# Kernel optimization log

Measured on AMD Instinct MI355X. Metric: run time of the kernel, lower is better.

## Reference

```python
import jax, jax.numpy as jnp
import numpy as np

WINDOW = 1024
HOP = 256

def setup_inputs() -> dict:
    key = jax.random.key(0)
    X = jax.random.normal(key, (16, 2, 262144), dtype=jnp.float32)
    return {"X": X}

def reference(X):
    # X: (B, 2, T) with channel 0 = Re, channel 1 = Im.
    # Identity-weight Conv1d(1, window, kernel=window, stride=hop) is exactly
    # strided framing: frame t is X[..., t*hop : t*hop + window].
    B, _, T = X.shape
    n_frames = (T - WINDOW) // HOP + 1
    # (n_frames, WINDOW) gather index into the time axis
    idx = jnp.arange(n_frames)[:, None] * HOP + jnp.arange(WINDOW)[None, :]
    frames = X[:, :, idx]                      # (B, 2, n_frames, WINDOW)
    return jnp.transpose(frames, (0, 1, 3, 2)) # (B, 2, WINDOW, n_frames)
```

## Files before the change

kernel.cpp:

```cpp
#include <hip/hip_runtime.h>

#define WINDOW_SZ 1024
#define HOP_SZ    256
#define NFRAMES   1021
#define T_LEN     262144

#define FT 256
#define WT 16
#define LDS_S 261

__global__ __launch_bounds__(256)
void frame_transpose2(const float* __restrict__ X, float* __restrict__ out) {
    __shared__ __align__(16) float lds[WT * LDS_S];

    const int tid  = threadIdx.x;
    const int f0   = blockIdx.x * FT;
    const int w0   = blockIdx.y * WT;
    const int bc   = blockIdx.z;
    const int flim = min(FT, NFRAMES - f0);

    const float* Xb = X + (size_t)bc * T_LEN;

    {
        const int q  = tid & 3;
        const int fr = tid >> 2;
#pragma unroll
        for (int p = 0; p < 4; ++p) {
            const int f = fr + 64 * p;
            if (f < flim) {
                const float4 v = *(const float4*)(Xb + (size_t)(f0 + f) * HOP_SZ + w0 + 4 * q);
                float* dst = &lds[(4 * q) * LDS_S + f];
                dst[0 * LDS_S] = v.x;
                dst[1 * LDS_S] = v.y;
                dst[2 * LDS_S] = v.z;
                dst[3 * LDS_S] = v.w;
            }
        }
    }
    __syncthreads();

    {
        const int lane = tid & 63;
        const int wv   = tid >> 6;
#pragma unroll
        for (int i = 0; i < 4; ++i) {
            const int wl = wv * 4 + i;
            const int wg = w0 + wl;
            const int p  = (4 - (wg & 3)) & 3;
            float* orow = out + ((size_t)bc * WINDOW_SZ + wg) * (size_t)NFRAMES + f0;
            const float* lrow = &lds[wl * LDS_S];

            const int fv = p + 4 * lane;
            if (fv + 4 <= flim) {
                const float4 v = *(const float4*)(lrow + fv);
                *(float4*)(orow + fv) = v;
            }
            const int nt = (flim - p) & 3;
            const int ts = flim - nt;
            int fs = -1;
            if (lane < p) fs = lane;
            else if (lane < p + nt) fs = ts + (lane - p);
            if (fs >= 0) orow[fs] = lrow[fs];
        }
    }
}

extern "C" void kernel_launch(void* const* d_in, const int* in_sizes, int n_in,
                              void* d_out, int out_size, void* d_ws, size_t ws_size,
                              hipStream_t stream) {
    const float* X = (const float*)d_in[0];
    float* out = (float*)d_out;

    dim3 block(256, 1, 1);
    dim3 grid((NFRAMES + FT - 1) / FT,
              WINDOW_SZ / WT,
              32);
    frame_transpose2<<<grid, block, 0, stream>>>(X, out);
}
```

Baseline: 173.1 us.

## Loop over frame chunks inside each block with wider window tile

Each block now owns a 32-wide window slice for one batch-channel and loops over all frames in chunks of 256, staging each chunk through LDS with two barriers per chunk. The window tile doubles from 16 to 32, so reads are 128-byte rows instead of 64-byte ones, and the grid shrinks from 8192 blocks to 1024. Fewer, longer blocks cut launch and tail overhead but leave less parallelism for hiding memory latency, and the in-loop barriers serialise loads and stores within a block.

```diff
diff --git a/kernel.cpp b/kernel.cpp
--- a/kernel.cpp
+++ b/kernel.cpp
@@ -5,55 +5,53 @@
 #define NFRAMES   1021
 #define T_LEN     262144
 
-#define FT 256
-#define WT 16
+#define WT 32
+#define FC 256
 #define LDS_S 261
 
 __global__ __launch_bounds__(256)
-void frame_transpose2(const float* __restrict__ X, float* __restrict__ out) {
+void frame_transpose3(const float* __restrict__ X, float* __restrict__ out) {
     __shared__ __align__(16) float lds[WT * LDS_S];
 
     const int tid  = threadIdx.x;
-    const int f0   = blockIdx.x * FT;
-    const int w0   = blockIdx.y * WT;
-    const int bc   = blockIdx.z;
-    const int flim = min(FT, NFRAMES - f0);
+    const int w0   = blockIdx.x * WT;
+    const int bc   = blockIdx.y;
 
-    const float* Xb = X + (size_t)bc * T_LEN;
+    const float* Xb = X + (size_t)bc * T_LEN + w0;
+    float* Ob = out + ((size_t)bc * WINDOW_SZ + w0) * (size_t)NFRAMES;
 
-    {
-        const int q  = tid & 3;
-        const int fr = tid >> 2;
+    const int j    = tid & 7;
+    const int fb   = tid >> 3;
+    const int lane = tid & 63;
+    const int wv   = tid >> 6;
+
+    for (int fc = 0; fc < NFRAMES; fc += FC) {
+        const int flim = min(FC, NFRAMES - fc);
+
 #pragma unroll
-        for (int p = 0; p < 4; ++p) {
-            const int f = fr + 64 * p;
+        for (int p = 0; p < 8; ++p) {
+            const int f = fb + 32 * p;
             if (f < flim) {
-                const float4 v = *(const float4*)(Xb + (size_t)(f0 + f) * HOP_SZ + w0 + 4 * q);
-                float* dst = &lds[(4 * q) * LDS_S + f];
+                const float4 v = *(const float4*)(Xb + (size_t)(fc + f) * HOP_SZ + 4 * j);
+                float* dst = &lds[(4 * j) * LDS_S + f];
                 dst[0 * LDS_S] = v.x;
                 dst[1 * LDS_S] = v.y;
                 dst[2 * LDS_S] = v.z;
                 dst[3 * LDS_S] = v.w;
             }
         }
-    }
-    __syncthreads();
+        __syncthreads();
 
-    {
-        const int lane = tid & 63;
-        const int wv   = tid >> 6;
 #pragma unroll
-        for (int i = 0; i < 4; ++i) {
-            const int wl = wv * 4 + i;
-            const int wg = w0 + wl;
-            const int p  = (4 - (wg & 3)) & 3;
-            float* orow = out + ((size_t)bc * WINDOW_SZ + wg) * (size_t)NFRAMES + f0;
-            const float* lrow = &lds[wl * LDS_S];
+        for (int r = 0; r < 8; ++r) {
+            const int w = wv * 8 + r;
+            const int p = (4 - ((w0 + w) & 3)) & 3;
+            float* orow = Ob + (size_t)w * NFRAMES + fc;
+            const float* lrow = &lds[w * LDS_S];
 
             const int fv = p + 4 * lane;
             if (fv + 4 <= flim) {
-                const float4 v = *(const float4*)(lrow + fv);
-                *(float4*)(orow + fv) = v;
+                *(float4*)(orow + fv) = *(const float4*)(lrow + fv);
             }
             const int nt = (flim - p) & 3;
             const int ts = flim - nt;
@@ -62,6 +60,7 @@
             else if (lane < p + nt) fs = ts + (lane - p);
             if (fs >= 0) orow[fs] = lrow[fs];
         }
+        __syncthreads();
     }
 }
 
@@ -72,8 +71,8 @@
     float* out = (float*)d_out;
 
     dim3 block(256, 1, 1);
-    dim3 grid((NFRAMES + FT - 1) / FT,
-              WINDOW_SZ / WT,
-              32);
-    frame_transpose2<<<grid, block, 0, stream>>>(X, out);
+    dim3 grid(WINDOW_SZ / WT,
+              32,
+              1);
+    frame_transpose3<<<grid, block, 0, stream>>>(X, out);
 }
```

After: 175.3 us. About the same (+1.3%).
